# Optimization experiments

Measured on AMD Instinct MI355X. Metric: run time of the kernel, lower is better.

## Reference

```python
import jax, jax.numpy as jnp
import numpy as np

N_NODES = 100000
N_EDGES = 1600000


def _gcn_norm(edge_index, num_nodes):
    """PyG gcn_norm: add self-loops, symmetric D^{-1/2} A_hat D^{-1/2} weights."""
    src, dst = edge_index[0], edge_index[1]
    loop = jnp.arange(num_nodes, dtype=edge_index.dtype)
    src = jnp.concatenate([src, loop])
    dst = jnp.concatenate([dst, loop])
    deg = jax.ops.segment_sum(jnp.ones_like(dst, dtype=jnp.float32), dst,
                              num_segments=num_nodes)
    dis = jnp.where(deg > 0, jax.lax.rsqrt(deg), 0.0)  # deg^{-1/2}, inf->0
    norm = dis[src] * dis[dst]  # [E+N]
    return src, dst, norm


def _gcn_conv(x, src, dst, norm, W, b, num_nodes):
    h = x @ W                              # [N, out] linear transform first
    msg = h[src] * norm[:, None]           # gather + normalize, [E+N, out]
    out = jax.ops.segment_sum(msg, dst, num_segments=num_nodes)  # scatter-add
    return out + b                         # PyG adds bias after aggregation


def setup_inputs() -> dict:
    key = jax.random.key(0)
    k1, k2, k3, k4 = jax.random.split(key, 4)
    x = jax.random.normal(k1, (N_NODES, 128), dtype=jnp.float32)
    edge_index = jax.random.randint(k2, (2, N_EDGES), 0, N_NODES, dtype=jnp.int64)
    # Glorot-style scaled weights
    W1 = jax.random.normal(k3, (128, 48), dtype=jnp.float32) * (1.0 / np.sqrt(128))
    b1 = jnp.zeros((48,), dtype=jnp.float32)
    W2 = jax.random.normal(k4, (48, 32), dtype=jnp.float32) * (1.0 / np.sqrt(48))
    b2 = jnp.zeros((32,), dtype=jnp.float32)
    return {"x": x, "edge_index": edge_index, "W1": W1, "b1": b1, "W2": W2, "b2": b2}


def reference(x, edge_index, W1, b1, W2, b2):
    n = x.shape[0]
    src, dst, norm = _gcn_norm(edge_index, n)
    z = jax.nn.relu(_gcn_conv(x, src, dst, norm, W1, b1, n))
    z = _gcn_conv(z, src, dst, norm, W2, b2, n)
    return z
```

## Files before the change

kernel.cpp:

```cpp
#include <hip/hip_runtime.h>


#define IN_DIM 128
#define H_DIM 48
#define O_DIM 32

__device__ __forceinline__ int clampi(int v, int hi) {
    return v < 0 ? 0 : (v >= hi ? hi - 1 : v);
}


__global__ void k_zero_i32(int* __restrict__ p, int n) {
    int i = blockIdx.x * blockDim.x + threadIdx.x;
    if (i < n) p[i] = 0;
}

__global__ void k_count(const int* __restrict__ dst, int* __restrict__ cnt,
                        int E, int N) {
    int e = blockIdx.x * blockDim.x + threadIdx.x;
    if (e < E) atomicAdd(&cnt[clampi(dst[e], N)], 1);
}

__global__ __launch_bounds__(1024) void k_scan1(const int* __restrict__ cnt,
                                                int* __restrict__ rp,
                                                int* __restrict__ bsum, int n) {
    __shared__ int sh[1024];
    const int tid = threadIdx.x;
    const int i = blockIdx.x * 1024 + tid;
    int v = (i < n) ? cnt[i] : 0;
    sh[tid] = v;
    __syncthreads();
    for (int off = 1; off < 1024; off <<= 1) {
        int t = (tid >= off) ? sh[tid - off] : 0;
        __syncthreads();
        sh[tid] += t;
        __syncthreads();
    }
    if (i < n) rp[i] = sh[tid] - v;
    if (tid == 1023) bsum[blockIdx.x] = sh[1023];
}

__global__ __launch_bounds__(128) void k_scan2(int* __restrict__ bsum, int nb) {
    __shared__ int sh[128];
    const int tid = threadIdx.x;
    int v = (tid < nb) ? bsum[tid] : 0;
    sh[tid] = v;
    __syncthreads();
    for (int off = 1; off < 128; off <<= 1) {
        int t = (tid >= off) ? sh[tid - off] : 0;
        __syncthreads();
        sh[tid] += t;
        __syncthreads();
    }
    if (tid < nb) bsum[tid] = sh[tid] - v;
}

__global__ void k_scan3(int* __restrict__ rp, const int* __restrict__ bsum,
                        int* __restrict__ cur, const int* __restrict__ cnt,
                        float* __restrict__ dis, int n, int E) {
    int i = blockIdx.x * blockDim.x + threadIdx.x;
    if (i < n) {
        int r = rp[i] + bsum[i >> 10];
        rp[i] = r;
        cur[i] = r;
        dis[i] = rsqrtf(1.0f + (float)cnt[i]);
    }
    if (i == 0) rp[n] = E;
}

__global__ void k_fill(const int* __restrict__ src, const int* __restrict__ dst,
                       const float* __restrict__ dis, int* __restrict__ cur,
                       int2* __restrict__ srt, int E, int N) {
    int e = blockIdx.x * blockDim.x + threadIdx.x;
    if (e >= E) return;
    int s = clampi(src[e], N);
    int d = clampi(dst[e], N);
    int p = atomicAdd(&cur[d], 1);
    srt[p] = make_int2(s, __float_as_int(dis[s]));
}


template <int K, int NO>
__global__ __launch_bounds__(256) void k_gemm(const float* __restrict__ X,
                                              const float* __restrict__ W,
                                              float* __restrict__ H, int n) {
    constexpr int BM = 32;
    constexpr int JPT = NO / 8;
    __shared__ float xs[BM * (K + 1)];
    __shared__ float ws[K * NO];

    const int t = threadIdx.x;
    const int node0 = blockIdx.x * BM;

    for (int i = t; i < K * NO; i += 256) ws[i] = W[i];
    for (int i = t; i < BM * K; i += 256) {
        int r = i / K, k = i % K;
        int node = node0 + r;
        xs[r * (K + 1) + k] = (node < n) ? X[(long long)node * K + k] : 0.0f;
    }
    __syncthreads();

    const int r = t >> 3;
    const int g = t & 7;
    float acc[JPT];
#pragma unroll
    for (int jj = 0; jj < JPT; jj++) acc[jj] = 0.0f;

    for (int k = 0; k < K; k++) {
        float xv = xs[r * (K + 1) + k];
#pragma unroll
        for (int jj = 0; jj < JPT; jj++) acc[jj] += xv * ws[k * NO + g * JPT + jj];
    }

    int node = node0 + r;
    if (node < n) {
#pragma unroll
        for (int jj = 0; jj < JPT; jj++)
            H[(long long)node * NO + g * JPT + jj] = acc[jj];
    }
}


template <int F, bool RELU>
__global__ __launch_bounds__(256) void k_pull(const int2* __restrict__ srt,
                                              const int* __restrict__ rp,
                                              const float* __restrict__ dis,
                                              const float* __restrict__ hbuf,
                                              const float* __restrict__ bias,
                                              float* __restrict__ out, int N) {
    const int w = blockIdx.x * 4 + (threadIdx.x >> 6);
    if (w >= N) return;
    const int lane = threadIdx.x & 63;
    const int beg = rp[w];
    const int end = rp[w + 1];
    const float disd = dis[w];
    float acc = 0.0f;

    if (F == 48) {
        const int j = lane;
        if (j < F) {
            int e = beg;
            for (; e + 1 < end; e += 2) {
                int2 p0 = srt[e];
                int2 p1 = srt[e + 1];
                float v0 = hbuf[(size_t)p0.x * F + j];
                float v1 = hbuf[(size_t)p1.x * F + j];
                acc = fmaf(v0, __int_as_float(p0.y) * disd, acc);
                acc = fmaf(v1, __int_as_float(p1.y) * disd, acc);
            }
            if (e < end) {
                int2 p = srt[e];
                acc = fmaf(hbuf[(size_t)p.x * F + j], __int_as_float(p.y) * disd, acc);
            }
            float val = acc + hbuf[(size_t)w * F + j] * disd * disd + bias[j];
            if (RELU) val = fmaxf(val, 0.0f);
            out[(size_t)w * F + j] = val;
        }
    } else {
        const int j = lane & 31;
        const int half = lane >> 5;
        for (int e = beg + half; e < end; e += 2) {
            int2 p = srt[e];
            acc = fmaf(hbuf[(size_t)p.x * F + j], __int_as_float(p.y) * disd, acc);
        }
        acc += __shfl_xor(acc, 32);
        if (lane < 32) {
            float val = acc + hbuf[(size_t)w * F + j] * disd * disd + bias[j];
            if (RELU) val = fmaxf(val, 0.0f);
            out[(size_t)w * F + j] = val;
        }
    }
}


__global__ void k_init_deg(float* __restrict__ deg, int n) {
    int i = blockIdx.x * blockDim.x + threadIdx.x;
    if (i < n) deg[i] = 1.0f;
}

__global__ void k_deg_edges(const int* __restrict__ dst, float* __restrict__ deg,
                            int E, int N) {
    int e = blockIdx.x * blockDim.x + threadIdx.x;
    if (e < E) unsafeAtomicAdd(&deg[clampi(dst[e], N)], 1.0f);
}

__global__ void k_rsqrt_inplace(float* __restrict__ d, int n) {
    int i = blockIdx.x * blockDim.x + threadIdx.x;
    if (i < n) d[i] = rsqrtf(d[i]);
}

template <int F, bool BIAS>
__global__ void k_selfloop_init(const float* __restrict__ h, const float* __restrict__ dis,
                                const float* __restrict__ bias, float* __restrict__ out,
                                int total) {
    int i = blockIdx.x * blockDim.x + threadIdx.x;
    if (i >= total) return;
    int n = i / F;
    float d = dis[n];
    float v = h[i] * d * d;
    if (BIAS) v += bias[i % F];
    out[i] = v;
}

template <int F>
__global__ void k_agg(const int* __restrict__ src, const int* __restrict__ dst,
                      const float* __restrict__ dis, const float* __restrict__ h,
                      float* __restrict__ out, unsigned total, int N) {
    unsigned t = blockIdx.x * blockDim.x + threadIdx.x;
    if (t >= total) return;
    unsigned e = t / F;
    unsigned j = t - e * F;
    int s = clampi(src[e], N);
    int d = clampi(dst[e], N);
    float v = h[(long long)s * F + j] * (dis[s] * dis[d]);
    unsafeAtomicAdd(&out[(long long)d * F + j], v);
}

__global__ void k_bias_relu(float* __restrict__ z, const float* __restrict__ b, int total) {
    int i = blockIdx.x * blockDim.x + threadIdx.x;
    if (i >= total) return;
    z[i] = fmaxf(z[i] + b[i % H_DIM], 0.0f);
}


static inline unsigned cdiv(unsigned a, unsigned b) { return (a + b - 1) / b; }

extern "C" void kernel_launch(void* const* d_in, const int* in_sizes, int n_in,
                              void* d_out, int out_size, void* d_ws, size_t ws_size,
                              hipStream_t stream) {
    const float* x = (const float*)d_in[0];
    const int* ei = (const int*)d_in[1];
    const float* W1 = (const float*)d_in[2];
    const float* b1 = (const float*)d_in[3];
    const float* W2 = (const float*)d_in[4];
    const float* b2 = (const float*)d_in[5];
    float* out = (float*)d_out;

    const int N = in_sizes[0] / IN_DIM;
    const int E = in_sizes[1] / 2;
    const int* src = ei;
    const int* dst = ei + E;
    const int NB = (int)cdiv(N, 1024);

    const int B = 256;
    char* base = (char*)d_ws;

    size_t off = 0;
    auto carve = [&](size_t bytes) { size_t o = off; off = (off + bytes + 255) & ~(size_t)255; return o; };
    size_t o_dis  = carve((size_t)N * 4);
    size_t o_cnt  = carve((size_t)N * 4);
    size_t o_rp   = carve(((size_t)N + 1) * 4);
    size_t o_cur  = carve((size_t)N * 4);
    size_t o_bsum = carve(256 * 4);
    size_t o_srt  = carve((size_t)E * 8);
    size_t o_h    = carve((size_t)N * H_DIM * 4);
    size_t o_z    = carve((size_t)N * H_DIM * 4);
    size_t need_pull = off;

    if (ws_size >= need_pull && NB <= 128) {
        float* dis = (float*)(base + o_dis);
        int*   cnt = (int*)(base + o_cnt);
        int*   rp  = (int*)(base + o_rp);
        int*   cur = (int*)(base + o_cur);
        int*   bsm = (int*)(base + o_bsum);
        int2*  srt = (int2*)(base + o_srt);
        float* h   = (float*)(base + o_h);
        float* z   = (float*)(base + o_z);
        float* h2  = h;

        k_zero_i32<<<cdiv(N, B), B, 0, stream>>>(cnt, N);
        k_count<<<cdiv(E, B), B, 0, stream>>>(dst, cnt, E, N);
        k_scan1<<<NB, 1024, 0, stream>>>(cnt, rp, bsm, N);
        k_scan2<<<1, 128, 0, stream>>>(bsm, NB);
        k_scan3<<<cdiv(N, B), B, 0, stream>>>(rp, bsm, cur, cnt, dis, N, E);
        k_fill<<<cdiv(E, B), B, 0, stream>>>(src, dst, dis, cur, srt, E, N);

        k_gemm<IN_DIM, H_DIM><<<cdiv(N, 32), B, 0, stream>>>(x, W1, h, N);
        k_pull<H_DIM, true><<<cdiv(N, 4), B, 0, stream>>>(srt, rp, dis, h, b1, z, N);

        k_gemm<H_DIM, O_DIM><<<cdiv(N, 32), B, 0, stream>>>(z, W2, h2, N);
        k_pull<O_DIM, false><<<cdiv(N, 4), B, 0, stream>>>(srt, rp, dis, h2, b2, out, N);
        return;
    }

    auto align_up = [](size_t v) { return (v + 63) & ~(size_t)63; };
    size_t f_dis = 0;
    size_t f_h   = f_dis + align_up((size_t)N);
    size_t f_z   = f_h + align_up((size_t)N * H_DIM);
    size_t need_push = (f_z + align_up((size_t)N * H_DIM)) * sizeof(float);
    if (ws_size < need_push) return;

    float* dis = (float*)d_ws + f_dis;
    float* h   = (float*)d_ws + f_h;
    float* z   = (float*)d_ws + f_z;
    float* h2  = h;

    k_init_deg<<<cdiv(N, B), B, 0, stream>>>(dis, N);
    k_deg_edges<<<cdiv(E, B), B, 0, stream>>>(dst, dis, E, N);
    k_rsqrt_inplace<<<cdiv(N, B), B, 0, stream>>>(dis, N);

    k_gemm<IN_DIM, H_DIM><<<cdiv(N, 32), B, 0, stream>>>(x, W1, h, N);
    k_selfloop_init<H_DIM, false><<<cdiv(N * H_DIM, B), B, 0, stream>>>(h, dis, b1, z, N * H_DIM);
    k_agg<H_DIM><<<cdiv((unsigned)E * H_DIM, B), B, 0, stream>>>(src, dst, dis, h, z, (unsigned)E * H_DIM, N);
    k_bias_relu<<<cdiv(N * H_DIM, B), B, 0, stream>>>(z, b1, N * H_DIM);

    k_gemm<H_DIM, O_DIM><<<cdiv(N, 32), B, 0, stream>>>(z, W2, h2, N);
    k_selfloop_init<O_DIM, true><<<cdiv(N * O_DIM, B), B, 0, stream>>>(h2, dis, b2, out, N * O_DIM);
    k_agg<O_DIM><<<cdiv((unsigned)E * O_DIM, B), B, 0, stream>>>(src, dst, dis, h2, out, (unsigned)E * O_DIM, N);
}
```

Before: 535.5 us.

## Replace random CSR fill with two-pass bucketed scatter by destination

Edges are first scattered into coarse buckets of 64 destination nodes, then a second pass scatters from these bucket-ordered edges into the final CSR slots. The aim is to make the atomics on per-node cursors and the CSR writes more localized, cutting the cost of fully random scatter. It adds a second histogram, an extra scan, and an extra pass over the edges, with the bucket buffer aliased onto the z buffer. The pull kernel also moves the destination normalization factor out of the per-edge loop.

```diff
diff --git a/kernel.cpp b/kernel.cpp
--- a/kernel.cpp
+++ b/kernel.cpp
@@ -4,6 +4,7 @@
 #define IN_DIM 128
 #define H_DIM 48
 #define O_DIM 32
+#define BKT_SHIFT 6
 
 __device__ __forceinline__ int clampi(int v, int hi) {
     return v < 0 ? 0 : (v >= hi ? hi - 1 : v);
@@ -15,19 +16,22 @@
     if (i < n) p[i] = 0;
 }
 
-__global__ void k_count(const int* __restrict__ dst, int* __restrict__ cnt,
-                        int E, int N) {
+__global__ void k_hist(const int* __restrict__ dst, int* __restrict__ cnt,
+                       int* __restrict__ bhist, int E, int N) {
     int e = blockIdx.x * blockDim.x + threadIdx.x;
-    if (e < E) atomicAdd(&cnt[clampi(dst[e], N)], 1);
-}
-
-__global__ __launch_bounds__(1024) void k_scan1(const int* __restrict__ cnt,
-                                                int* __restrict__ rp,
+    if (e >= E) return;
+    int d = clampi(dst[e], N);
+    atomicAdd(&cnt[d], 1);
+    atomicAdd(&bhist[d >> BKT_SHIFT], 1);
+}
+
+__global__ __launch_bounds__(1024) void k_scan1(const int* __restrict__ in,
+                                                int* __restrict__ out,
                                                 int* __restrict__ bsum, int n) {
     __shared__ int sh[1024];
     const int tid = threadIdx.x;
     const int i = blockIdx.x * 1024 + tid;
-    int v = (i < n) ? cnt[i] : 0;
+    int v = (i < n) ? in[i] : 0;
     sh[tid] = v;
     __syncthreads();
     for (int off = 1; off < 1024; off <<= 1) {
@@ -36,7 +40,7 @@
         sh[tid] += t;
         __syncthreads();
     }
-    if (i < n) rp[i] = sh[tid] - v;
+    if (i < n) out[i] = sh[tid] - v;
     if (tid == 1023) bsum[blockIdx.x] = sh[1023];
 }
 
@@ -68,15 +72,34 @@
     if (i == 0) rp[n] = E;
 }
 
-__global__ void k_fill(const int* __restrict__ src, const int* __restrict__ dst,
-                       const float* __restrict__ dis, int* __restrict__ cur,
-                       int2* __restrict__ srt, int E, int N) {
+__global__ void k_bfix(int* __restrict__ boff, const int* __restrict__ bsum2,
+                       int* __restrict__ bcur, int nb) {
+    int i = blockIdx.x * blockDim.x + threadIdx.x;
+    if (i < nb) {
+        int r = boff[i] + bsum2[i >> 10];
+        boff[i] = r;
+        bcur[i] = r;
+    }
+}
+
+__global__ void k_passA(const int* __restrict__ src, const int* __restrict__ dst,
+                        int* __restrict__ bcur, int2* __restrict__ buck,
+                        int E, int N) {
     int e = blockIdx.x * blockDim.x + threadIdx.x;
     if (e >= E) return;
     int s = clampi(src[e], N);
     int d = clampi(dst[e], N);
-    int p = atomicAdd(&cur[d], 1);
-    srt[p] = make_int2(s, __float_as_int(dis[s]));
+    int p = atomicAdd(&bcur[d >> BKT_SHIFT], 1);
+    buck[p] = make_int2(s, d);
+}
+
+__global__ void k_passB(const int2* __restrict__ buck, const float* __restrict__ dis,
+                        int* __restrict__ cur, int2* __restrict__ srt, int E) {
+    int i = blockIdx.x * blockDim.x + threadIdx.x;
+    if (i >= E) return;
+    int2 sd = buck[i];
+    int p = atomicAdd(&cur[sd.y], 1);
+    srt[p] = make_int2(sd.x, __float_as_int(dis[sd.x]));
 }
 
 
@@ -145,14 +168,14 @@
                 int2 p1 = srt[e + 1];
                 float v0 = hbuf[(size_t)p0.x * F + j];
                 float v1 = hbuf[(size_t)p1.x * F + j];
-                acc = fmaf(v0, __int_as_float(p0.y) * disd, acc);
-                acc = fmaf(v1, __int_as_float(p1.y) * disd, acc);
+                acc = fmaf(v0, __int_as_float(p0.y), acc);
+                acc = fmaf(v1, __int_as_float(p1.y), acc);
             }
             if (e < end) {
                 int2 p = srt[e];
-                acc = fmaf(hbuf[(size_t)p.x * F + j], __int_as_float(p.y) * disd, acc);
+                acc = fmaf(hbuf[(size_t)p.x * F + j], __int_as_float(p.y), acc);
             }
-            float val = acc + hbuf[(size_t)w * F + j] * disd * disd + bias[j];
+            float val = (acc + hbuf[(size_t)w * F + j] * disd) * disd + bias[j];
             if (RELU) val = fmaxf(val, 0.0f);
             out[(size_t)w * F + j] = val;
         }
@@ -161,11 +184,11 @@
         const int half = lane >> 5;
         for (int e = beg + half; e < end; e += 2) {
             int2 p = srt[e];
-            acc = fmaf(hbuf[(size_t)p.x * F + j], __int_as_float(p.y) * disd, acc);
+            acc = fmaf(hbuf[(size_t)p.x * F + j], __int_as_float(p.y), acc);
         }
         acc += __shfl_xor(acc, 32);
         if (lane < 32) {
-            float val = acc + hbuf[(size_t)w * F + j] * disd * disd + bias[j];
+            float val = (acc + hbuf[(size_t)w * F + j] * disd) * disd + bias[j];
             if (RELU) val = fmaxf(val, 0.0f);
             out[(size_t)w * F + j] = val;
         }
@@ -240,40 +263,60 @@
     const int E = in_sizes[1] / 2;
     const int* src = ei;
     const int* dst = ei + E;
-    const int NB = (int)cdiv(N, 1024);
+    const int NB   = (int)cdiv(N, 1024);
+    const int NBKT = (N + (1 << BKT_SHIFT) - 1) >> BKT_SHIFT;
+    const int NB2  = (int)cdiv(NBKT, 1024);
 
     const int B = 256;
     char* base = (char*)d_ws;
 
     size_t off = 0;
     auto carve = [&](size_t bytes) { size_t o = off; off = (off + bytes + 255) & ~(size_t)255; return o; };
-    size_t o_dis  = carve((size_t)N * 4);
-    size_t o_cnt  = carve((size_t)N * 4);
-    size_t o_rp   = carve(((size_t)N + 1) * 4);
-    size_t o_cur  = carve((size_t)N * 4);
-    size_t o_bsum = carve(256 * 4);
-    size_t o_srt  = carve((size_t)E * 8);
-    size_t o_h    = carve((size_t)N * H_DIM * 4);
-    size_t o_z    = carve((size_t)N * H_DIM * 4);
+    size_t o_dis   = carve((size_t)N * 4);
+    size_t o_cnt   = carve((size_t)N * 4);
+    size_t o_rp    = carve(((size_t)N + 1) * 4);
+    size_t o_cur   = carve((size_t)N * 4);
+    size_t o_bsum  = carve(256 * 4);
+    size_t o_bsum2 = carve(256 * 4);
+    size_t o_bhist = carve((size_t)NBKT * 4);
+    size_t o_boff  = carve((size_t)NBKT * 4);
+    size_t o_bcur  = carve((size_t)NBKT * 4);
+    size_t o_srt   = carve((size_t)E * 8);
+    size_t o_h     = carve((size_t)N * H_DIM * 4);
+    size_t o_z     = carve((size_t)N * H_DIM * 4);
     size_t need_pull = off;
-
-    if (ws_size >= need_pull && NB <= 128) {
-        float* dis = (float*)(base + o_dis);
-        int*   cnt = (int*)(base + o_cnt);
-        int*   rp  = (int*)(base + o_rp);
-        int*   cur = (int*)(base + o_cur);
-        int*   bsm = (int*)(base + o_bsum);
-        int2*  srt = (int2*)(base + o_srt);
-        float* h   = (float*)(base + o_h);
-        float* z   = (float*)(base + o_z);
-        float* h2  = h;
+    bool buck_fits = (size_t)E * 8 <= (size_t)N * H_DIM * 4;
+
+    if (ws_size >= need_pull && NB <= 128 && NB2 <= 128 && buck_fits) {
+        float* dis  = (float*)(base + o_dis);
+        int*   cnt  = (int*)(base + o_cnt);
+        int*   rp   = (int*)(base + o_rp);
+        int*   cur  = (int*)(base + o_cur);
+        int*   bsm  = (int*)(base + o_bsum);
+        int*   bsm2 = (int*)(base + o_bsum2);
+        int*   bhist= (int*)(base + o_bhist);
+        int*   boff = (int*)(base + o_boff);
+        int*   bcur = (int*)(base + o_bcur);
+        int2*  srt  = (int2*)(base + o_srt);
+        float* h    = (float*)(base + o_h);
+        float* z    = (float*)(base + o_z);
+        int2*  buck = (int2*)(base + o_z);
+        float* h2   = h;
 
         k_zero_i32<<<cdiv(N, B), B, 0, stream>>>(cnt, N);
-        k_count<<<cdiv(E, B), B, 0, stream>>>(dst, cnt, E, N);
+        k_zero_i32<<<cdiv(NBKT, B), B, 0, stream>>>(bhist, NBKT);
+        k_hist<<<cdiv(E, B), B, 0, stream>>>(dst, cnt, bhist, E, N);
+
         k_scan1<<<NB, 1024, 0, stream>>>(cnt, rp, bsm, N);
         k_scan2<<<1, 128, 0, stream>>>(bsm, NB);
         k_scan3<<<cdiv(N, B), B, 0, stream>>>(rp, bsm, cur, cnt, dis, N, E);
-        k_fill<<<cdiv(E, B), B, 0, stream>>>(src, dst, dis, cur, srt, E, N);
+
+        k_scan1<<<NB2, 1024, 0, stream>>>(bhist, boff, bsm2, NBKT);
+        k_scan2<<<1, 128, 0, stream>>>(bsm2, NB2);
+        k_bfix<<<cdiv(NBKT, B), B, 0, stream>>>(boff, bsm2, bcur, NBKT);
+
+        k_passA<<<cdiv(E, B), B, 0, stream>>>(src, dst, bcur, buck, E, N);
+        k_passB<<<cdiv(E, B), B, 0, stream>>>(buck, dis, cur, srt, E);
 
         k_gemm<IN_DIM, H_DIM><<<cdiv(N, 32), B, 0, stream>>>(x, W1, h, N);
         k_pull<H_DIM, true><<<cdiv(N, 4), B, 0, stream>>>(srt, rp, dis, h, b1, z, N);
```

After: 961.2 us. 1.8x slower.
